# Performance work log

Hardware: AMD Instinct MI355X
Metric: run time of the kernel (lower is better)

## Reference

```python
import jax, jax.numpy as jnp
import numpy as np
from math import floor, log2

DEPTH = 4
DIM = 1024
HEADS = 16
DIM_HEAD = 64
FF_MULT = 4
NUM_TOKENS = 32000
SEQ = 2048
MASK_VALUE = -1e10
EPS = 1e-5
ATTN_INNER = DIM_HEAD * HEADS            # 1024
FF_INNER = DIM * FF_MULT                 # 4096
FUSED = (ATTN_INNER, DIM_HEAD, DIM_HEAD, FF_INNER, FF_INNER)  # q, k, v, ff, ff_gate


def get_alibi_slopes(heads):
    def pow2_slopes(n):
        start = 2 ** (-2 ** (-(log2(n) - 3)))
        return [start * start ** i for i in range(n)]
    if log2(heads).is_integer():
        return pow2_slopes(heads)
    c = 2 ** floor(log2(heads))
    return pow2_slopes(c) + pow2_slopes(2 * c)[0::2][: heads - c]


def make_attn_bias(seq_len, heads, mask_value):
    # ALiBi variant used by this module: bias depends only on key position j
    slopes = np.array(get_alibi_slopes(heads), dtype=np.float32)[:, None, None]  # [h,1,1]
    bias = slopes * np.arange(seq_len, dtype=np.float32)[None, None, :]          # [h,1,j]
    bias = np.broadcast_to(bias, (heads, seq_len, seq_len))
    causal = np.tril(np.ones((seq_len, seq_len), dtype=bool))
    return jnp.asarray(np.where(causal, bias, mask_value), dtype=jnp.float32)


def rmsnorm(x, gamma):
    ssq = jnp.sum(jnp.square(x), axis=-1, keepdims=True)
    return jax.lax.rsqrt(ssq + EPS) * x * gamma * (x.shape[-1] ** 0.5)


def block(x, attn_bias, wi, attn_wo, ff_wo, gamma):
    h = rmsnorm(x, gamma)
    splits = np.cumsum(FUSED[:-1])
    q, k, v, ff, ff_gate = jnp.split(h @ wi, splits, axis=-1)
    b, n, _ = q.shape
    # multi-query attention: k, v have a single shared head of size DIM_HEAD
    q = q.reshape(b, n, HEADS, DIM_HEAD).transpose(0, 2, 1, 3) * (DIM_HEAD ** -0.5)
    sim = jnp.einsum('bhid,bjd->bhij', q, k) + attn_bias
    attn = jax.nn.softmax(sim, axis=-1)
    out = jnp.einsum('bhij,bjd->bhid', attn, v)
    out = out.transpose(0, 2, 1, 3).reshape(b, n, ATTN_INNER)
    attn_out = out @ attn_wo
    ff_out = (ff * jax.nn.swish(ff_gate)) @ ff_wo
    return attn_out + ff_out


def setup_inputs() -> dict:
    key = jax.random.key(0)
    ks = jax.random.split(key, 6)
    return {
        'tokens': jax.random.randint(ks[0], (1, SEQ), 0, NUM_TOKENS),
        'embedding': jax.random.normal(ks[1], (NUM_TOKENS, DIM), jnp.float32) * 0.02,
        'wi': jax.random.normal(ks[2], (DEPTH, DIM, sum(FUSED)), jnp.float32),
        'attn_wo': jax.random.normal(ks[3], (DEPTH, ATTN_INNER, DIM), jnp.float32),
        'ff_wo': jax.random.normal(ks[4], (DEPTH, FF_INNER, DIM), jnp.float32),
        'gammas': jnp.ones((DEPTH, DIM), jnp.float32),
        'final_gamma': jnp.ones((DIM,), jnp.float32),
    }


def reference(tokens, embedding, wi, attn_wo, ff_wo, gammas, final_gamma):
    n = tokens.shape[-1]
    attn_bias = make_attn_bias(SEQ, HEADS, MASK_VALUE)[..., :n, :n]
    x = embedding[tokens]                     # [b, n, dim]
    for l in range(DEPTH):
        x = block(x, attn_bias, wi[l], attn_wo[l], ff_wo[l], gammas[l]) + x
    x = rmsnorm(x, final_gamma)
    return x @ embedding.T                    # tied-embedding logits [b, n, vocab]
```

## Files before the change

### kernel.cpp

```cpp
#include <hip/hip_runtime.h>
#include <stdint.h>


typedef __attribute__((ext_vector_type(8))) __bf16 bf16x8;
typedef __attribute__((ext_vector_type(4))) __bf16 bf16x4;
typedef __attribute__((ext_vector_type(8))) short s16x8;
typedef __attribute__((ext_vector_type(4))) float f32x4;

#define SEQ   2048
#define DIM   1024
#define NHEAD 16
#define DHEAD 64
#define FUSEN 9344
#define QKW   1088
#define FFIN  4096
#define VOCAB 32000
#define AFW   5120
#define LOG2E 1.44269504f

__device__ __forceinline__ f32x4 mfma16(bf16x8 a, bf16x8 b, f32x4 c) {
  return __builtin_amdgcn_mfma_f32_16x16x32_bf16(
      __builtin_bit_cast(s16x8, a), __builtin_bit_cast(s16x8, b), c, 0, 0, 0);
}

__device__ __forceinline__ void load_lds16(const __bf16* g, __bf16* l) {
  __builtin_amdgcn_global_load_lds(
      (const __attribute__((address_space(1))) uint32_t*)g,
      (__attribute__((address_space(3))) uint32_t*)l, 16, 0, 0);
}


__global__ void cast_k(const float* __restrict__ in, __bf16* __restrict__ out, int n8) {
  int i = blockIdx.x * 256 + threadIdx.x;
  if (i >= n8) return;
  const float4* p = (const float4*)in + (size_t)i * 2;
  float4 a = p[0], b = p[1];
  bf16x8 o;
  o[0] = (__bf16)a.x; o[1] = (__bf16)a.y; o[2] = (__bf16)a.z; o[3] = (__bf16)a.w;
  o[4] = (__bf16)b.x; o[5] = (__bf16)b.y; o[6] = (__bf16)b.z; o[7] = (__bf16)b.w;
  *(bf16x8*)(out + (size_t)i * 8) = o;
}

__device__ __forceinline__ int permcol(int c) {
  if (c < 1152) return c;
  if (c < 5248) { int i = c - 1152; return 1152 + ((i >> 4) << 5) + (i & 15); }
  int i = c - 5248; return 1152 + ((i >> 4) << 5) + 16 + (i & 15);
}

__global__ __launch_bounds__(256) void transpose_wi_k(
    const float* __restrict__ in, __bf16* __restrict__ out) {
  __shared__ float tile[64][65];
  int l = blockIdx.z;
  int tx = threadIdx.x & 63, ty = threadIdx.x >> 6;
  int c0 = blockIdx.x * 64, r0 = blockIdx.y * 64;
  const float* inl = in + (size_t)l * DIM * FUSEN;
  __bf16* outl = out + (size_t)l * FUSEN * DIM;
  for (int i = ty; i < 64; i += 4)
    tile[i][tx] = inl[(size_t)(r0 + i) * FUSEN + c0 + tx];
  __syncthreads();
  for (int i = ty; i < 64; i += 4)
    outl[(size_t)permcol(c0 + i) * DIM + r0 + tx] = (__bf16)tile[tx][i];
}

__global__ __launch_bounds__(256) void transpose_b_k(
    const float* __restrict__ in, __bf16* __restrict__ out,
    int R, int C, int ldo, int co, size_t outLstride) {
  __shared__ float tile[64][65];
  int l = blockIdx.z;
  int tx = threadIdx.x & 63, ty = threadIdx.x >> 6;
  int c0 = blockIdx.x * 64, r0 = blockIdx.y * 64;
  const float* inl = in + (size_t)l * R * C;
  __bf16* outl = out + (size_t)l * outLstride;
  for (int i = ty; i < 64; i += 4)
    tile[i][tx] = inl[(size_t)(r0 + i) * C + c0 + tx];
  __syncthreads();
  for (int i = ty; i < 64; i += 4)
    outl[(size_t)(c0 + i) * ldo + co + r0 + tx] = (__bf16)tile[tx][i];
}

template <int MODE>
__global__ __launch_bounds__(256) void rmsnorm_fuse_k(
    const float* __restrict__ x, const float* __restrict__ p,
    const int* __restrict__ tokens, const float* __restrict__ emb,
    const float* __restrict__ gamma, float* __restrict__ xn,
    __bf16* __restrict__ h) {
  int n = blockIdx.x;
  float4 v;
  if (MODE == 0) {
    int tok = tokens[n];
    v = ((const float4*)(emb + (size_t)tok * DIM))[threadIdx.x];
    ((float4*)(xn + (size_t)n * DIM))[threadIdx.x] = v;
  } else {
    v = ((const float4*)(x + (size_t)n * DIM))[threadIdx.x];
    float4 a = ((const float4*)(p + (size_t)n * DIM))[threadIdx.x];
    float4 b = ((const float4*)(p + (size_t)(SEQ + n) * DIM))[threadIdx.x];
    v.x += a.x + b.x; v.y += a.y + b.y; v.z += a.z + b.z; v.w += a.w + b.w;
    ((float4*)(xn + (size_t)n * DIM))[threadIdx.x] = v;
  }
  float ssq = v.x * v.x + v.y * v.y + v.z * v.z + v.w * v.w;
  for (int m = 32; m >= 1; m >>= 1) ssq += __shfl_xor(ssq, m, 64);
  __shared__ float red[4];
  if ((threadIdx.x & 63) == 0) red[threadIdx.x >> 6] = ssq;
  __syncthreads();
  float tot = red[0] + red[1] + red[2] + red[3];
  float rs = rsqrtf(tot + 1e-5f) * 32.0f;
  float4 g = ((const float4*)gamma)[threadIdx.x];
  bf16x4 o;
  o[0] = (__bf16)(v.x * rs * g.x);
  o[1] = (__bf16)(v.y * rs * g.y);
  o[2] = (__bf16)(v.z * rs * g.z);
  o[3] = (__bf16)(v.w * rs * g.w);
  *(bf16x4*)(h + (size_t)n * DIM + threadIdx.x * 4) = o;
}

template <int MODE>
__global__ __launch_bounds__(256) void gemm_bt_k(
    const __bf16* __restrict__ A, int lda,
    const __bf16* __restrict__ Bt, int ldb,
    float* __restrict__ outf, int ldc,
    __bf16* __restrict__ qh, __bf16* __restrict__ ql,
    __bf16* __restrict__ vT, __bf16* __restrict__ aof,
    int K) {
  __shared__ __bf16 lA[8192];
  __shared__ __bf16 lB[8192];
  const int t = threadIdx.x;
  const int lane = t & 63, wave = t >> 6;
  const int lo4 = lane & 15, hi2 = lane >> 4;
  const int nwg = gridDim.x * gridDim.y;
  const int orig = blockIdx.y * gridDim.x + blockIdx.x;
  const int xcd = orig & 7, off = orig >> 3;
  const int qq = nwg >> 3, rr = nwg & 7;
  const int nid = (xcd < rr ? xcd * (qq + 1) : rr * (qq + 1) + (xcd - rr) * qq) + off;
  const int bm = nid % gridDim.y, bn = nid / gridDim.y;
  const int k0 = blockIdx.z * K;
  const int wr = (wave >> 1) * 64, wc = (wave & 1) * 64;

  f32x4 acc[4][4];
#pragma unroll
  for (int m = 0; m < 4; m++)
#pragma unroll
    for (int n = 0; n < 4; n++) acc[m][n] = f32x4{0.f, 0.f, 0.f, 0.f};

  const int e0 = t * 8;
  const int e1 = 2048 + t * 8;
  const __bf16* gA0 = A + (size_t)(bm * 128 + (e0 >> 5)) * lda + (e0 & 31) + k0;
  const __bf16* gA1 = A + (size_t)(bm * 128 + (e1 >> 5)) * lda + (e1 & 31) + k0;
  const __bf16* gB0 = Bt + (size_t)(bn * 128 + (e0 >> 5)) * ldb + (e0 & 31) + k0;
  const __bf16* gB1 = Bt + (size_t)(bn * 128 + (e1 >> 5)) * ldb + (e1 & 31) + k0;
  __bf16* dA0 = &lA[wave * 512];
  __bf16* dA1 = &lA[2048 + wave * 512];
  __bf16* dB0 = &lB[wave * 512];
  __bf16* dB1 = &lB[2048 + wave * 512];

  for (int kt = 0; kt < K; kt += 64) {
    load_lds16(gA0 + kt, dA0);
    load_lds16(gA1 + kt, dA1);
    load_lds16(gB0 + kt, dB0);
    load_lds16(gB1 + kt, dB1);
    load_lds16(gA0 + kt + 32, dA0 + 4096);
    load_lds16(gA1 + kt + 32, dA1 + 4096);
    load_lds16(gB0 + kt + 32, dB0 + 4096);
    load_lds16(gB1 + kt + 32, dB1 + 4096);
    __syncthreads();
#pragma unroll
    for (int half = 0; half < 2; half++) {
      const __bf16* sA = &lA[half * 4096];
      const __bf16* sB = &lB[half * 4096];
      bf16x8 af[4], bf_[4];
#pragma unroll
      for (int m = 0; m < 4; m++)
        af[m] = *(const bf16x8*)&sA[(wr + m * 16 + lo4) * 32 + hi2 * 8];
#pragma unroll
      for (int n = 0; n < 4; n++)
        bf_[n] = *(const bf16x8*)&sB[(wc + n * 16 + lo4) * 32 + hi2 * 8];
#pragma unroll
      for (int m = 0; m < 4; m++)
#pragma unroll
        for (int n = 0; n < 4; n++)
          acc[m][n] = mfma16(af[m], bf_[n], acc[m][n]);
    }
    __syncthreads();
  }

  if (MODE == 0) {
    float* op = outf + (size_t)blockIdx.z * SEQ * DIM;
#pragma unroll
    for (int m = 0; m < 4; m++) {
      const int rowb = bm * 128 + wr + m * 16 + hi2 * 4;
#pragma unroll
      for (int n = 0; n < 4; n++) {
        const int col = bn * 128 + wc + n * 16 + lo4;
#pragma unroll
        for (int j = 0; j < 4; j++)
          __builtin_nontemporal_store(acc[m][n][j], &op[(size_t)(rowb + j) * ldc + col]);
      }
    }
  } else if (bn < 8 || (bn == 8 && wc == 0)) {
#pragma unroll
    for (int m = 0; m < 4; m++) {
      const int rowb = bm * 128 + wr + m * 16 + hi2 * 4;
#pragma unroll
      for (int n = 0; n < 4; n++) {
        const int col = bn * 128 + wc + n * 16 + lo4;
#pragma unroll
        for (int j = 0; j < 4; j++) {
          float v = acc[m][n][j];
          __bf16 hi = (__bf16)v;
          qh[(size_t)(rowb + j) * QKW + col] = hi;
          ql[(size_t)(rowb + j) * QKW + col] = (__bf16)(v - (float)hi);
        }
      }
    }
  } else if (bn == 8) {
#pragma unroll
    for (int m = 0; m < 4; m++) {
      const int rowb = bm * 128 + wr + m * 16 + hi2 * 4;
#pragma unroll
      for (int n = 0; n < 4; n++) {
        const int vcol = n * 16 + lo4;
#pragma unroll
        for (int j = 0; j < 4; j++)
          vT[(size_t)vcol * SEQ + rowb + j] = (__bf16)acc[m][n][j];
      }
    }
  } else {
#pragma unroll
    for (int m = 0; m < 4; m++) {
      const int rowb = bm * 128 + wr + m * 16 + hi2 * 4;
#pragma unroll
      for (int np = 0; np < 4; np += 2) {
        const int cb = (bn - 9) * 128 + wc + np * 16;
        const int acol = 1024 + ((cb >> 5) << 4) + lo4;
#pragma unroll
        for (int j = 0; j < 4; j++) {
          float ff = acc[m][np][j];
          float gg = acc[m][np + 1][j];
          float s = gg / (1.f + expf(-gg));
          aof[(size_t)(rowb + j) * AFW + acol] = (__bf16)(ff * s);
        }
      }
    }
  }
}

__global__ __launch_bounds__(512, 1) void gemm256_k(
    const __bf16* __restrict__ A, const __bf16* __restrict__ Bt,
    float* __restrict__ C, int ldc, int K) {
  __shared__ __bf16 lds[65536];
  const int t = threadIdx.x;
  const int lane = t & 63, w = t >> 6;
  const int lo4 = lane & 15, hi2 = lane >> 4;
  const int wr = w >> 2, wc = w & 3;
  const int nwg = gridDim.x * gridDim.y;
  const int orig = blockIdx.y * gridDim.x + blockIdx.x;
  const int xcd = orig & 7, off = orig >> 3;
  const int qq = nwg >> 3, rr = nwg & 7;
  const int nid = (xcd < rr ? xcd * (qq + 1) : rr * (qq + 1) + (xcd - rr) * qq) + off;
  const int bm = nid % gridDim.y, bn = nid / gridDim.y;

  const int srow = lane >> 2;
  const int scol = ((lane & 3) * 8) ^ ((lane >> 5) << 4);
  const __bf16* gA = A + (size_t)(bm * 256 + srow) * K + scol;
  const __bf16* gB = Bt + (size_t)(bn * 256 + srow) * K + scol;
  const int cpr = (hi2 * 8) ^ ((lo4 >= 8) ? 16 : 0);

  auto STAGE = [&](int kt, int ks, int isB) {
    const __bf16* g = (isB ? gB : gA) + kt * 64 + ks * 32;
    __bf16* l = &lds[isB * 32768 + (kt & 1) * 16384 + ks * 8192 + (2 * w) * 512];
    load_lds16(g + (size_t)(2 * w) * 16 * K, l);
    load_lds16(g + (size_t)(2 * w + 1) * 16 * K, l + 512);
  };

  f32x4 acc[8][4];
#pragma unroll
  for (int m = 0; m < 8; m++)
#pragma unroll
    for (int n = 0; n < 4; n++) acc[m][n] = f32x4{0.f, 0.f, 0.f, 0.f};

  STAGE(0, 0, 0); STAGE(0, 0, 1); STAGE(0, 1, 0); STAGE(0, 1, 1);

  const int NIT = K >> 7;
  bf16x8 bfr[4];
  for (int it = 0; it < NIT; ++it) {
#pragma unroll
    for (int p = 0; p < 8; ++p) {
      const int g = p >> 2;
      const int u = p & 3;
      const int ks = u >> 1, mh = u & 1;
      const int kt = 2 * it + g;
      const bool dostage = (it < NIT - 1) || (g == 0);
      if ((u & 1) == 0) {
        if (it == NIT - 1 && g == 1 && u == 2)
          asm volatile("s_waitcnt vmcnt(0)" ::: "memory");
        else
          asm volatile("s_waitcnt vmcnt(4)" ::: "memory");
        __builtin_amdgcn_s_barrier();
      }
      const int abase = g * 16384 + ks * 8192 + lo4 * 32 + cpr;
      if ((u & 1) == 0) {
#pragma unroll
        for (int n = 0; n < 4; n++)
          bfr[n] = *(const bf16x8*)&lds[32768 + abase + (wc * 4 + n) * 512];
      }
      bf16x8 af[4];
#pragma unroll
      for (int mm = 0; mm < 4; mm++)
        af[mm] = *(const bf16x8*)&lds[abase + (wr * 8 + mh * 4 + mm) * 512];
      if (dostage) STAGE(kt + 1, ks, u & 1);
      __builtin_amdgcn_s_setprio(1);
#pragma unroll
      for (int mm = 0; mm < 4; mm++)
#pragma unroll
        for (int n = 0; n < 4; n++)
          acc[mh * 4 + mm][n] = mfma16(af[mm], bfr[n], acc[mh * 4 + mm][n]);
      __builtin_amdgcn_s_setprio(0);
    }
  }

#pragma unroll
  for (int m = 0; m < 8; m++) {
    const int rowb = bm * 256 + wr * 128 + m * 16 + hi2 * 4;
#pragma unroll
    for (int n = 0; n < 4; n++) {
      const int col = bn * 256 + wc * 64 + n * 16 + lo4;
#pragma unroll
      for (int j = 0; j < 4; j++)
        __builtin_nontemporal_store(acc[m][n][j], &C[(size_t)(rowb + j) * ldc + col]);
    }
  }
}

__global__ __launch_bounds__(256, 4) void flash_k(
    const __bf16* __restrict__ qh, const __bf16* __restrict__ ql,
    const __bf16* __restrict__ vT, __bf16* __restrict__ aof) {
  const int t = threadIdx.x;
  const int lane = t & 63, wave = t >> 6;
  const int lo4 = lane & 15, hi2 = lane >> 4;
  const int b = blockIdx.x;
  const int h = b & 15;
  const int s = b >> 4;
  const int pr = wave >> 1, half = wave & 1;
  const int c = pr ? (127 - s) : s;
  const int qrow0 = c * 16;
  const int nt = (c >> 2) + 1;
  const int ntA = (nt + 1) >> 1;
  const int jt0 = half ? ntA : 0;
  const int jtE = half ? nt : ntA;
  const float slope2 = exp2f(-0.5f * (float)(h + 1)) * LOG2E;
  const float scale2 = 0.125f * LOG2E;

  __shared__ __bf16 lP[4][16][72];
  __shared__ float smO[2][2][16][65];
  __shared__ float sml[2][2][16][2];
  __bf16 (*lPw)[72] = lP[wave];

  bf16x8 qhf[2], qlf[2];
#pragma unroll
  for (int kk = 0; kk < 2; kk++) {
    size_t qoff = (size_t)(qrow0 + lo4) * QKW + h * 64 + kk * 32 + hi2 * 8;
    qhf[kk] = *(const bf16x8*)(qh + qoff);
    qlf[kk] = *(const bf16x8*)(ql + qoff);
  }

  float jb[4][4];
#pragma unroll
  for (int f = 0; f < 4; f++)
#pragma unroll
    for (int r = 0; r < 4; r++)
      jb[f][r] = slope2 * (float)(jt0 * 64 + f * 16 + hi2 * 4 + r);
  const float dj = slope2 * 64.0f;
  const int iq = qrow0 + lo4;

  f32x4 O[4];
#pragma unroll
  for (int f = 0; f < 4; f++) O[f] = f32x4{0.f, 0.f, 0.f, 0.f};
  float mr = -1e30f, lr = 0.f;

  for (int jt = jt0; jt < jtE; ++jt) {
    f32x4 sc[4];
#pragma unroll
    for (int f = 0; f < 4; f++) sc[f] = f32x4{0.f, 0.f, 0.f, 0.f};
    __builtin_amdgcn_s_setprio(1);
#pragma unroll
    for (int kk = 0; kk < 2; kk++) {
#pragma unroll
      for (int f = 0; f < 4; f++) {
        size_t koff = (size_t)(jt * 64 + f * 16 + lo4) * QKW + 1024 + kk * 32 + hi2 * 8;
        bf16x8 khf = *(const bf16x8*)(qh + koff);
        bf16x8 klf = *(const bf16x8*)(ql + koff);
        sc[f] = mfma16(khf, qlf[kk], sc[f]);
        sc[f] = mfma16(klf, qhf[kk], sc[f]);
        sc[f] = mfma16(khf, qhf[kk], sc[f]);
      }
    }
    __builtin_amdgcn_s_setprio(0);

    float pv[4][4];
    float tmax = -1e30f;
#pragma unroll
    for (int f = 0; f < 4; f++)
#pragma unroll
      for (int r = 0; r < 4; r++) {
        const int j = jt * 64 + f * 16 + hi2 * 4 + r;
        float v = fmaf(sc[f][r], scale2, jb[f][r]);
        if (j > iq) v = -1e30f;
        pv[f][r] = v;
        tmax = fmaxf(tmax, v);
      }
    tmax = fmaxf(tmax, __shfl_xor(tmax, 16, 64));
    tmax = fmaxf(tmax, __shfl_xor(tmax, 32, 64));
    float mn = fmaxf(mr, tmax);
    float corr = exp2f(mr - mn);
    mr = mn;
    float rs = 0.f;
#pragma unroll
    for (int f = 0; f < 4; f++)
#pragma unroll
      for (int r = 0; r < 4; r++) {
        float pe = exp2f(pv[f][r] - mn);
        __bf16 pb = (__bf16)pe;
        lPw[lo4][f * 16 + hi2 * 4 + r] = pb;
        rs += (float)pb;
      }
    rs += __shfl_xor(rs, 16, 64);
    rs += __shfl_xor(rs, 32, 64);
    lr = lr * corr + rs;
    float co[4];
#pragma unroll
    for (int r = 0; r < 4; r++)
      co[r] = __shfl(corr, (lane & 48) + hi2 * 4 + r, 64);
#pragma unroll
    for (int f = 0; f < 4; f++)
#pragma unroll
      for (int r = 0; r < 4; r++) O[f][r] *= co[r];

    __builtin_amdgcn_s_setprio(1);
#pragma unroll
    for (int kk = 0; kk < 2; kk++) {
      bf16x8 pa = *(const bf16x8*)&lPw[lo4][kk * 32 + hi2 * 8];
#pragma unroll
      for (int f = 0; f < 4; f++) {
        bf16x8 vb = *(const bf16x8*)(vT + (size_t)(f * 16 + lo4) * SEQ + jt * 64 + kk * 32 + hi2 * 8);
        O[f] = mfma16(pa, vb, O[f]);
      }
    }
    __builtin_amdgcn_s_setprio(0);

#pragma unroll
    for (int f = 0; f < 4; f++)
#pragma unroll
      for (int r = 0; r < 4; r++) jb[f][r] += dj;
  }

#pragma unroll
  for (int f = 0; f < 4; f++)
#pragma unroll
    for (int r = 0; r < 4; r++)
      smO[pr][half][hi2 * 4 + r][f * 16 + lo4] = O[f][r];
  if (hi2 == 0) {
    sml[pr][half][lo4][0] = mr;
    sml[pr][half][lo4][1] = lr;
  }
  __syncthreads();
  if (half == 0) {
#pragma unroll
    for (int r = 0; r < 4; r++) {
      const int row = hi2 * 4 + r;
      float mA = sml[pr][0][row][0], lA = sml[pr][0][row][1];
      float mB = sml[pr][1][row][0], lB = sml[pr][1][row][1];
      float mS = fmaxf(mA, mB);
      float cA = exp2f(mA - mS), cB = exp2f(mB - mS);
      float li = lA * cA + lB * cB;
#pragma unroll
      for (int f = 0; f < 4; f++) {
        float v = (smO[pr][0][row][f * 16 + lo4] * cA +
                   smO[pr][1][row][f * 16 + lo4] * cB) / li;
        aof[(size_t)(qrow0 + row) * AFW + h * 64 + f * 16 + lo4] = (__bf16)v;
      }
    }
  }
}


extern "C" void kernel_launch(void* const* d_in, const int* in_sizes, int n_in,
                              void* d_out, int out_size, void* d_ws, size_t ws_size,
                              hipStream_t stream) {
  const int* tokens  = (const int*)d_in[0];
  const float* emb   = (const float*)d_in[1];
  const float* wi    = (const float*)d_in[2];
  const float* awo   = (const float*)d_in[3];
  const float* fwo   = (const float*)d_in[4];
  const float* gam   = (const float*)d_in[5];
  const float* fgam  = (const float*)d_in[6];
  float* out = (float*)d_out;

  char* wsp = (char*)d_ws;
  size_t woff = 0;
  auto walloc = [&](size_t b) { void* p = wsp + woff; woff += (b + 255) & ~(size_t)255; return p; };
  __bf16* embb = (__bf16*)walloc((size_t)VOCAB * DIM * 2);
  __bf16* h    = (__bf16*)walloc((size_t)SEQ * DIM * 2);

  char* op = (char*)d_out;
  size_t ooff = 0;
  auto oalloc = [&](size_t b) { void* p = op + ooff; ooff += (b + 255) & ~(size_t)255; return p; };
  float*  xA    = (float*)oalloc((size_t)SEQ * DIM * 4);
  float*  xB    = (float*)oalloc((size_t)SEQ * DIM * 4);
  float*  pp    = (float*)oalloc((size_t)2 * SEQ * DIM * 4);
  __bf16* qhb   = (__bf16*)oalloc((size_t)SEQ * QKW * 2);
  __bf16* qlb   = (__bf16*)oalloc((size_t)SEQ * QKW * 2);
  __bf16* vT    = (__bf16*)oalloc((size_t)DHEAD * SEQ * 2);
  __bf16* aof   = (__bf16*)oalloc((size_t)SEQ * AFW * 2);
  __bf16* wiT4  = (__bf16*)oalloc((size_t)4 * FUSEN * DIM * 2);
  __bf16* BT24  = (__bf16*)oalloc((size_t)4 * DIM * AFW * 2);
  (void)ws_size; (void)in_sizes; (void)n_in; (void)out_size;

  cast_k<<<(VOCAB * DIM / 8 + 255) / 256, 256, 0, stream>>>(emb, embb, VOCAB * DIM / 8);
  transpose_wi_k<<<dim3(FUSEN / 64, DIM / 64, 4), 256, 0, stream>>>(wi, wiT4);
  transpose_b_k<<<dim3(DIM / 64, DIM / 64, 4), 256, 0, stream>>>(
      awo, BT24, DIM, DIM, AFW, 0, (size_t)DIM * AFW);
  transpose_b_k<<<dim3(DIM / 64, FFIN / 64, 4), 256, 0, stream>>>(
      fwo, BT24, FFIN, DIM, AFW, 1024, (size_t)DIM * AFW);

  float* x = xA;
  float* xn = xB;
  for (int l = 0; l < 4; l++) {
    if (l == 0) {
      rmsnorm_fuse_k<0><<<SEQ, 256, 0, stream>>>(
          nullptr, nullptr, tokens, emb, gam, x, h);
    } else {
      rmsnorm_fuse_k<1><<<SEQ, 256, 0, stream>>>(
          x, pp, nullptr, nullptr, gam + l * DIM, xn, h);
      float* tmp = x; x = xn; xn = tmp;
    }
    gemm_bt_k<1><<<dim3(FUSEN / 128, SEQ / 128), 256, 0, stream>>>(
        h, DIM, wiT4 + (size_t)l * FUSEN * DIM, DIM, nullptr, 0,
        qhb, qlb, vT, aof, DIM);
    flash_k<<<dim3(1024), 256, 0, stream>>>(qhb, qlb, vT, aof);
    gemm_bt_k<0><<<dim3(DIM / 128, SEQ / 128, 2), 256, 0, stream>>>(
        aof, AFW, BT24 + (size_t)l * DIM * AFW, AFW, pp, DIM,
        nullptr, nullptr, nullptr, nullptr, AFW / 2);
  }

  rmsnorm_fuse_k<1><<<SEQ, 256, 0, stream>>>(
      x, pp, nullptr, nullptr, fgam, xn, h);
  gemm256_k<<<dim3(VOCAB / 256, SEQ / 256), 512, 0, stream>>>(
      h, embb, out, VOCAB, DIM);
}
```

Measured before the change: 1.188 ms.

## Run fused QKV/FF projection on 256x256 GEMM kernel with fused epilogues

Moves the per-layer input projection from the 128x128-tile GEMM to the larger 256x256-tile, 512-thread GEMM. The weight is padded to 9472 columns, and the q/k split, vT and swiglu epilogues are ported to 64-column quads. The aim is more data reuse per workgroup and fewer workgroups. A new rmsnorm mode skips the unused residual write on the final norm. The cost is padded wasted columns and a smaller grid (37x8), which may underfill the CUs.

```diff
diff --git a/kernel.cpp b/kernel.cpp
--- a/kernel.cpp
+++ b/kernel.cpp
@@ -12,6 +12,7 @@
 #define NHEAD 16
 #define DHEAD 64
 #define FUSEN 9344
+#define WIN   9472
 #define QKW   1088
 #define FFIN  4096
 #define VOCAB 32000
@@ -54,7 +55,7 @@
   int tx = threadIdx.x & 63, ty = threadIdx.x >> 6;
   int c0 = blockIdx.x * 64, r0 = blockIdx.y * 64;
   const float* inl = in + (size_t)l * DIM * FUSEN;
-  __bf16* outl = out + (size_t)l * FUSEN * DIM;
+  __bf16* outl = out + (size_t)l * WIN * DIM;
   for (int i = ty; i < 64; i += 4)
     tile[i][tx] = inl[(size_t)(r0 + i) * FUSEN + c0 + tx];
   __syncthreads();
@@ -95,7 +96,8 @@
     float4 a = ((const float4*)(p + (size_t)n * DIM))[threadIdx.x];
     float4 b = ((const float4*)(p + (size_t)(SEQ + n) * DIM))[threadIdx.x];
     v.x += a.x + b.x; v.y += a.y + b.y; v.z += a.z + b.z; v.w += a.w + b.w;
-    ((float4*)(xn + (size_t)n * DIM))[threadIdx.x] = v;
+    if (MODE == 1)
+      ((float4*)(xn + (size_t)n * DIM))[threadIdx.x] = v;
   }
   float ssq = v.x * v.x + v.y * v.y + v.z * v.z + v.w * v.w;
   for (int m = 32; m >= 1; m >>= 1) ssq += __shfl_xor(ssq, m, 64);
@@ -113,14 +115,10 @@
   *(bf16x4*)(h + (size_t)n * DIM + threadIdx.x * 4) = o;
 }
 
-template <int MODE>
 __global__ __launch_bounds__(256) void gemm_bt_k(
     const __bf16* __restrict__ A, int lda,
     const __bf16* __restrict__ Bt, int ldb,
-    float* __restrict__ outf, int ldc,
-    __bf16* __restrict__ qh, __bf16* __restrict__ ql,
-    __bf16* __restrict__ vT, __bf16* __restrict__ aof,
-    int K) {
+    float* __restrict__ outf, int ldc, int K) {
   __shared__ __bf16 lA[8192];
   __shared__ __bf16 lB[8192];
   const int t = threadIdx.x;
@@ -182,70 +180,27 @@
     __syncthreads();
   }
 
-  if (MODE == 0) {
-    float* op = outf + (size_t)blockIdx.z * SEQ * DIM;
-#pragma unroll
-    for (int m = 0; m < 4; m++) {
-      const int rowb = bm * 128 + wr + m * 16 + hi2 * 4;
-#pragma unroll
-      for (int n = 0; n < 4; n++) {
-        const int col = bn * 128 + wc + n * 16 + lo4;
-#pragma unroll
-        for (int j = 0; j < 4; j++)
-          __builtin_nontemporal_store(acc[m][n][j], &op[(size_t)(rowb + j) * ldc + col]);
-      }
-    }
-  } else if (bn < 8 || (bn == 8 && wc == 0)) {
-#pragma unroll
-    for (int m = 0; m < 4; m++) {
-      const int rowb = bm * 128 + wr + m * 16 + hi2 * 4;
-#pragma unroll
-      for (int n = 0; n < 4; n++) {
-        const int col = bn * 128 + wc + n * 16 + lo4;
-#pragma unroll
-        for (int j = 0; j < 4; j++) {
-          float v = acc[m][n][j];
-          __bf16 hi = (__bf16)v;
-          qh[(size_t)(rowb + j) * QKW + col] = hi;
-          ql[(size_t)(rowb + j) * QKW + col] = (__bf16)(v - (float)hi);
-        }
-      }
-    }
-  } else if (bn == 8) {
-#pragma unroll
-    for (int m = 0; m < 4; m++) {
-      const int rowb = bm * 128 + wr + m * 16 + hi2 * 4;
-#pragma unroll
-      for (int n = 0; n < 4; n++) {
-        const int vcol = n * 16 + lo4;
-#pragma unroll
-        for (int j = 0; j < 4; j++)
-          vT[(size_t)vcol * SEQ + rowb + j] = (__bf16)acc[m][n][j];
-      }
-    }
-  } else {
-#pragma unroll
-    for (int m = 0; m < 4; m++) {
-      const int rowb = bm * 128 + wr + m * 16 + hi2 * 4;
-#pragma unroll
-      for (int np = 0; np < 4; np += 2) {
-        const int cb = (bn - 9) * 128 + wc + np * 16;
-        const int acol = 1024 + ((cb >> 5) << 4) + lo4;
-#pragma unroll
-        for (int j = 0; j < 4; j++) {
-          float ff = acc[m][np][j];
-          float gg = acc[m][np + 1][j];
-          float s = gg / (1.f + expf(-gg));
-          aof[(size_t)(rowb + j) * AFW + acol] = (__bf16)(ff * s);
-        }
-      }
-    }
-  }
-}
-
+  float* op = outf + (size_t)blockIdx.z * SEQ * DIM;
+#pragma unroll
+  for (int m = 0; m < 4; m++) {
+    const int rowb = bm * 128 + wr + m * 16 + hi2 * 4;
+#pragma unroll
+    for (int n = 0; n < 4; n++) {
+      const int col = bn * 128 + wc + n * 16 + lo4;
+#pragma unroll
+      for (int j = 0; j < 4; j++)
+        __builtin_nontemporal_store(acc[m][n][j], &op[(size_t)(rowb + j) * ldc + col]);
+    }
+  }
+}
+
+template <int MODE>
 __global__ __launch_bounds__(512, 1) void gemm256_k(
     const __bf16* __restrict__ A, const __bf16* __restrict__ Bt,
-    float* __restrict__ C, int ldc, int K) {
+    float* __restrict__ C, int ldc,
+    __bf16* __restrict__ qh, __bf16* __restrict__ ql,
+    __bf16* __restrict__ vT, __bf16* __restrict__ aof,
+    int K) {
   __shared__ __bf16 lds[65536];
   const int t = threadIdx.x;
   const int lane = t & 63, w = t >> 6;
@@ -317,15 +272,65 @@
     }
   }
 
-#pragma unroll
-  for (int m = 0; m < 8; m++) {
-    const int rowb = bm * 256 + wr * 128 + m * 16 + hi2 * 4;
-#pragma unroll
-    for (int n = 0; n < 4; n++) {
-      const int col = bn * 256 + wc * 64 + n * 16 + lo4;
-#pragma unroll
-      for (int j = 0; j < 4; j++)
-        __builtin_nontemporal_store(acc[m][n][j], &C[(size_t)(rowb + j) * ldc + col]);
+  if (MODE == 0) {
+#pragma unroll
+    for (int m = 0; m < 8; m++) {
+      const int rowb = bm * 256 + wr * 128 + m * 16 + hi2 * 4;
+#pragma unroll
+      for (int n = 0; n < 4; n++) {
+        const int col = bn * 256 + wc * 64 + n * 16 + lo4;
+#pragma unroll
+        for (int j = 0; j < 4; j++)
+          __builtin_nontemporal_store(acc[m][n][j], &C[(size_t)(rowb + j) * ldc + col]);
+      }
+    }
+  } else {
+    const int quad = bn * 4 + wc;
+    if (quad < 17) {
+#pragma unroll
+      for (int m = 0; m < 8; m++) {
+        const int rowb = bm * 256 + wr * 128 + m * 16 + hi2 * 4;
+#pragma unroll
+        for (int n = 0; n < 4; n++) {
+          const int col = quad * 64 + n * 16 + lo4;
+#pragma unroll
+          for (int j = 0; j < 4; j++) {
+            float v = acc[m][n][j];
+            __bf16 hi = (__bf16)v;
+            qh[(size_t)(rowb + j) * QKW + col] = hi;
+            ql[(size_t)(rowb + j) * QKW + col] = (__bf16)(v - (float)hi);
+          }
+        }
+      }
+    } else if (quad == 17) {
+#pragma unroll
+      for (int m = 0; m < 8; m++) {
+        const int rowb = bm * 256 + wr * 128 + m * 16 + hi2 * 4;
+#pragma unroll
+        for (int n = 0; n < 4; n++) {
+          const int vcol = n * 16 + lo4;
+#pragma unroll
+          for (int j = 0; j < 4; j++)
+            vT[(size_t)vcol * SEQ + rowb + j] = (__bf16)acc[m][n][j];
+        }
+      }
+    } else if (quad < 146) {
+#pragma unroll
+      for (int m = 0; m < 8; m++) {
+        const int rowb = bm * 256 + wr * 128 + m * 16 + hi2 * 4;
+#pragma unroll
+        for (int np = 0; np < 4; np += 2) {
+          const int cb = quad * 64 - 1152 + np * 16;
+          const int acol = 1024 + ((cb >> 5) << 4) + lo4;
+#pragma unroll
+          for (int j = 0; j < 4; j++) {
+            float ff = acc[m][np][j];
+            float gg = acc[m][np + 1][j];
+            float s = gg / (1.f + expf(-gg));
+            aof[(size_t)(rowb + j) * AFW + acol] = (__bf16)(ff * s);
+          }
+        }
+      }
     }
   }
 }
@@ -510,7 +515,7 @@
   __bf16* qlb   = (__bf16*)oalloc((size_t)SEQ * QKW * 2);
   __bf16* vT    = (__bf16*)oalloc((size_t)DHEAD * SEQ * 2);
   __bf16* aof   = (__bf16*)oalloc((size_t)SEQ * AFW * 2);
-  __bf16* wiT4  = (__bf16*)oalloc((size_t)4 * FUSEN * DIM * 2);
+  __bf16* wiT4  = (__bf16*)oalloc((size_t)4 * WIN * DIM * 2);
   __bf16* BT24  = (__bf16*)oalloc((size_t)4 * DIM * AFW * 2);
   (void)ws_size; (void)in_sizes; (void)n_in; (void)out_size;
 
@@ -532,17 +537,15 @@
           x, pp, nullptr, nullptr, gam + l * DIM, xn, h);
       float* tmp = x; x = xn; xn = tmp;
     }
-    gemm_bt_k<1><<<dim3(FUSEN / 128, SEQ / 128), 256, 0, stream>>>(
-        h, DIM, wiT4 + (size_t)l * FUSEN * DIM, DIM, nullptr, 0,
-        qhb, qlb, vT, aof, DIM);
+    gemm256_k<1><<<dim3(WIN / 256, SEQ / 256), 512, 0, stream>>>(
+        h, wiT4 + (size_t)l * WIN * DIM, nullptr, 0, qhb, qlb, vT, aof, DIM);
     flash_k<<<dim3(1024), 256, 0, stream>>>(qhb, qlb, vT, aof);
-    gemm_bt_k<0><<<dim3(DIM / 128, SEQ / 128, 2), 256, 0, stream>>>(
-        aof, AFW, BT24 + (size_t)l * DIM * AFW, AFW, pp, DIM,
-        nullptr, nullptr, nullptr, nullptr, AFW / 2);
-  }
-
-  rmsnorm_fuse_k<1><<<SEQ, 256, 0, stream>>>(
-      x, pp, nullptr, nullptr, fgam, xn, h);
-  gemm256_k<<<dim3(VOCAB / 256, SEQ / 256), 512, 0, stream>>>(
-      h, embb, out, VOCAB, DIM);
-}
+    gemm_bt_k<<<dim3(DIM / 128, SEQ / 128, 2), 256, 0, stream>>>(
+        aof, AFW, BT24 + (size_t)l * DIM * AFW, AFW, pp, DIM, AFW / 2);
+  }
+
+  rmsnorm_fuse_k<2><<<SEQ, 256, 0, stream>>>(
+      x, pp, nullptr, nullptr, fgam, nullptr, h);
+  gemm256_k<0><<<dim3(VOCAB / 256, SEQ / 256), 512, 0, stream>>>(
+      h, embb, out, VOCAB, nullptr, nullptr, nullptr, nullptr, DIM);
+}
```

Result: no change. 1.207 ms (+1.5%).
